# Optimization experiments

Hardware: AMD Instinct MI355X
Metric: run time of the kernel (lower is better)

The kernel has to match this reference:

```python
import jax, jax.numpy as jnp
import numpy as np

K_NBR = 128        # PyG radius(max_num_neighbors=128)
NEG_FILL = -1e9    # mask value for max-aggregation over invalid neighbors


def fps(pos, m):
    # Farthest point sampling on pos [N,2] -> [m] int32 indices (start at 0).
    n = pos.shape[0]
    def step(carry, _):
        min_d2, last = carry
        d2 = jnp.sum((pos - pos[last]) ** 2, axis=-1)
        min_d2 = jnp.minimum(min_d2, d2)
        nxt = jnp.argmax(min_d2).astype(jnp.int32)
        return (min_d2, nxt), nxt
    init = (jnp.full((n,), 1e10, pos.dtype), jnp.int32(0))
    _, idxs = jax.lax.scan(step, init, None, length=m - 1)
    return jnp.concatenate([jnp.zeros((1,), jnp.int32), idxs])


def set_abstraction(x, pos, ratio, r, W, b):
    # x [B,N,C], pos [B,N,2]. FPS centers, radius neighbors (<=K), PointNetConv
    # message = Linear(cat[x_j, pos_j - pos_i]) (PyG MLP with one layer and
    # plain_last=True is a bare Linear), then max-aggregate per center.
    B, N, C = x.shape
    m = int(N * ratio)
    idx = jax.vmap(lambda p: fps(p, m))(pos)                         # [B,m]
    ctr = jnp.take_along_axis(pos, idx[..., None], axis=1)           # [B,m,2]
    d2 = jnp.sum((ctr[:, :, None, :] - pos[:, None, :, :]) ** 2, -1)  # [B,m,N]
    k = min(K_NBR, N)
    neg_d2, nbr = jax.lax.top_k(-d2, k)                              # [B,m,k]
    valid = (-neg_d2) <= r * r                                       # in-radius mask
    gather = jax.vmap(lambda a, i: a[i])                             # per-sample fancy index
    x_j = gather(x, nbr)                                             # [B,m,k,C]
    rel = gather(pos, nbr) - ctr[:, :, None, :]                      # [B,m,k,2]
    msg = jnp.concatenate([x_j, rel], axis=-1) @ W + b               # [B,m,k,F]
    msg = jnp.where(valid[..., None], msg, NEG_FILL)
    return jnp.max(msg, axis=2), ctr                                 # [B,m,F], [B,m,2]


def encoder(x, zones_ids, lf_W1, lf_b1, lf_W2, lf_b2, c1_W, c1_b, c2_W, c2_b, c3_W, c3_b):
    lf = jnp.tanh(jnp.tanh(x @ lf_W1 + lf_b1) @ lf_W2 + lf_b2)       # [B,N,64]
    h = jnp.concatenate([lf, zones_ids], axis=-1)                    # [B,N,65]
    h, pos = set_abstraction(h, x, 0.5, 0.5, c1_W, c1_b)             # [B,N/2,64]
    h, pos = set_abstraction(h, pos, 0.25, 1.0, c2_W, c2_b)          # [B,N/8,128]
    g = jnp.concatenate([h, pos], axis=-1) @ c3_W + c3_b             # [B,N/8,1024]
    gf = jnp.max(g, axis=1, keepdims=True)                           # global max pool -> [B,1,1024]
    return lf, gf


def setup_inputs():
    key = jax.random.key(0)
    ks = jax.random.split(key, 12)
    B, N = 4, 4096
    def lin(kw, kb, fi, fo):
        return (jax.random.normal(kw, (fi, fo), jnp.float32) / np.sqrt(fi),
                jax.random.normal(kb, (fo,), jnp.float32) * 0.01)
    x = jax.random.normal(ks[0], (B, N, 2), jnp.float32) * 4.0  # spread so ball(r) holds <128 pts
    zones_ids = jax.random.uniform(ks[1], (B, N, 1), jnp.float32)
    lf_W1, lf_b1 = lin(ks[2], ks[3], 2, 64)
    lf_W2, lf_b2 = lin(ks[4], ks[5], 64, 64)
    c1_W, c1_b = lin(ks[6], ks[7], 67, 64)
    c2_W, c2_b = lin(ks[8], ks[9], 66, 128)
    c3_W, c3_b = lin(ks[10], ks[11], 130, 1024)
    return {"x": x, "zones_ids": zones_ids, "lf_W1": lf_W1, "lf_b1": lf_b1,
            "lf_W2": lf_W2, "lf_b2": lf_b2, "c1_W": c1_W, "c1_b": c1_b,
            "c2_W": c2_W, "c2_b": c2_b, "c3_W": c3_W, "c3_b": c3_b}


def reference(x, zones_ids, lf_W1, lf_b1, lf_W2, lf_b2, c1_W, c1_b, c2_W, c2_b, c3_W, c3_b):
    return encoder(x, zones_ids, lf_W1, lf_b1, lf_W2, lf_b2,
                   c1_W, c1_b, c2_W, c2_b, c3_W, c3_b)
```

## Files before the change

### kernel.cpp

```cpp
#include <hip/hip_runtime.h>


constexpr int BB = 4;
constexpr int NN = 4096;
constexpr int M1 = 2048;
constexpr int M2 = 512;

typedef float v2f __attribute__((ext_vector_type(2)));

__device__ __forceinline__ float d2_exact(float dx, float dy) {
    return __fadd_rn(__fmul_rn(dx, dx), __fmul_rn(dy, dy));
}

template<int CTRL>
__device__ __forceinline__ unsigned long long dpp64z(unsigned long long v) {
    unsigned lo = (unsigned)__builtin_amdgcn_update_dpp(0, (int)(unsigned)v, CTRL, 0xF, 0xF, true);
    unsigned hi = (unsigned)__builtin_amdgcn_update_dpp(0, (int)(unsigned)(v >> 32), CTRL, 0xF, 0xF, true);
    return ((unsigned long long)hi << 32) | (unsigned long long)lo;
}
template<int CTRL>
__device__ __forceinline__ void pairc(unsigned long long& t1, unsigned long long& t2) {
    unsigned long long o1 = dpp64z<CTRL>(t1);
    unsigned long long o2 = dpp64z<CTRL>(t2);
    bool g = o1 > t1;
    unsigned long long m1 = g ? o1 : t1;
    unsigned long long sm = g ? t1 : o1;
    unsigned long long cn = g ? o2 : t2;
    t2 = cn > sm ? cn : sm;
    t1 = m1;
}

template<int M, int PPT>
__device__ __forceinline__ void fps_core(
    const float2* __restrict__ src, const float2* __restrict__ PTSl,
    float2* __restrict__ centl, uint4 (&slk)[2][4],
    int tid, int lane, int wv)
{
#pragma clang fp contract(off)
    constexpr int PP2 = PPT / 2;
    v2f px2[PP2], py2[PP2], md2[PP2];
#pragma unroll
    for (int k = 0; k < PP2; ++k) {
        float2 a = src[tid + (2 * k) * 256];
        float2 b = src[tid + (2 * k + 1) * 256];
        px2[k] = (v2f){a.x, b.x};
        py2[k] = (v2f){a.y, b.y};
        md2[k] = (v2f){1e10f, 1e10f};
    }
    float2 c0 = src[0];
    if (tid == 0) centl[0] = c0;

    unsigned baseu = 0xFFFFFFFFu - (unsigned)tid;
    float c1x = c0.x, c1y = c0.y, c2x = 0.0f, c2y = 0.0f;
    bool two = false;
    int it = 1;
    unsigned rc = 0;
    while (it < M) {
        int par = (int)(rc & 1u); ++rc;
        v2f vcx = (v2f){c1x, c1x}, vcy = (v2f){c1y, c1y};
#pragma unroll
        for (int k = 0; k < PP2; ++k) {
            v2f dx = px2[k] - vcx, dy = py2[k] - vcy;
            v2f d2 = (dx * dx) + (dy * dy);
            md2[k] = __builtin_elementwise_min(md2[k], d2);
        }
        if (two) {
            v2f wcx = (v2f){c2x, c2x}, wcy = (v2f){c2y, c2y};
#pragma unroll
            for (int k = 0; k < PP2; ++k) {
                v2f dx = px2[k] - wcx, dy = py2[k] - wcy;
                v2f d2 = (dx * dx) + (dy * dy);
                md2[k] = __builtin_elementwise_min(md2[k], d2);
            }
        }
        float t1f = -1.0f, t2f = -1.0f;
        unsigned i1 = 0u, i2 = 0u;
#pragma unroll
        for (int s = 0; s < PPT; ++s) {
            float mq = (s & 1) ? md2[s >> 1].y : md2[s >> 1].x;
            unsigned io = baseu - (unsigned)(s * 256);
            bool g1 = mq > t1f;
            bool g2 = mq > t2f;
            t2f = g1 ? t1f : (g2 ? mq : t2f);
            i2  = g1 ? i1  : (g2 ? io : i2);
            t1f = g1 ? mq : t1f;
            i1  = g1 ? io : i1;
        }
        unsigned long long t1 =
            ((unsigned long long)__float_as_uint(t1f) << 32) | (unsigned long long)i1;
        unsigned long long t2 =
            ((unsigned long long)__float_as_uint(t2f) << 32) | (unsigned long long)i2;
        pairc<0x111>(t1, t2); pairc<0x112>(t1, t2); pairc<0x114>(t1, t2);
        pairc<0x118>(t1, t2); pairc<0x142>(t1, t2); pairc<0x143>(t1, t2);
        if (lane == 63)
            slk[par][wv] = make_uint4((unsigned)t1, (unsigned)(t1 >> 32),
                                      (unsigned)t2, (unsigned)(t2 >> 32));
        __syncthreads();
        uint4 e = slk[par][lane & 3];
        unsigned long long a1 = ((unsigned long long)e.y << 32) | (unsigned long long)e.x;
        unsigned long long a2 = ((unsigned long long)e.w << 32) | (unsigned long long)e.z;
        pairc<0xB1>(a1, a2);
        pairc<0x4E>(a1, a2);
        int jw = (int)(0xFFFFFFFFu - (unsigned)a1);
        int jr = (int)(0xFFFFFFFFu - (unsigned)a2);
        float mdr = __uint_as_float((unsigned)(a2 >> 32));
        float2 wpt = PTSl[jw];
        float2 rpt = PTSl[jr];
        float ddx = rpt.x - wpt.x, ddy = rpt.y - wpt.y;
        float dd = (ddx * ddx) + (ddy * ddy);
        bool dbl = (it + 1 < M) && (dd >= mdr);
        if (tid == 0) { centl[it] = wpt; if (dbl) centl[it + 1] = rpt; }
        c1x = wpt.x; c1y = wpt.y; c2x = rpt.x; c2y = rpt.y;
        two = dbl;
        it += dbl ? 2 : 1;
    }
}

__global__ __launch_bounds__(256, 1) void k_fps_lf(
    const float2* __restrict__ pos, float* __restrict__ p1out,
    float* __restrict__ p2out,
    const float* __restrict__ zones,
    const float* __restrict__ W1, const float* __restrict__ b1,
    const float* __restrict__ W2, const float* __restrict__ b2,
    const float* __restrict__ c1W, const float* __restrict__ c1b,
    float* __restrict__ out_lf, float* __restrict__ y1)
{
    __shared__ float2 PTS[NN];
    __shared__ float2 cent1[M1];
    __shared__ float2 cent2[M2];
    __shared__ uint4 slk[2][4];
    int tid = threadIdx.x, lane = tid & 63, wv = tid >> 6;

    if (blockIdx.x >= (unsigned)BB) {
        float* sh = (float*)PTS;
        float* sl = sh + 256;
        int p = tid >> 6, f = tid & 63;
        size_t pt = (size_t)(blockIdx.x - BB) * 4 + p;
        float2 xv = pos[pt];
        float hid = tanhf(xv.x * W1[f] + xv.y * W1[64 + f] + b1[f]);
        sh[p * 64 + f] = hid;
        __syncthreads();
        float acc = b2[f];
#pragma unroll
        for (int c = 0; c < 64; ++c) acc += sh[p * 64 + c] * W2[c * 64 + f];
        float lf = tanhf(acc);
        sl[p * 64 + f] = lf;
        out_lf[pt * 64 + f] = lf;
        __syncthreads();
        float acc2 = c1b[f] + zones[pt] * c1W[64 * 64 + f]
                   + xv.x * c1W[65 * 64 + f] + xv.y * c1W[66 * 64 + f];
#pragma unroll
        for (int c = 0; c < 64; ++c) acc2 += sl[p * 64 + c] * c1W[c * 64 + f];
        y1[pt * 64 + f] = acc2;
        return;
    }

    const float2* p = pos + (size_t)blockIdx.x * NN;
    for (int i = tid; i < NN; i += 256) PTS[i] = p[i];
    __syncthreads();

    fps_core<M1, NN / 256>(p, PTS, cent1, slk, tid, lane, wv);
    __syncthreads();
    float2* o1 = (float2*)(p1out + (size_t)blockIdx.x * M1 * 2);
    for (int i = tid; i < M1; i += 256) o1[i] = cent1[i];

    fps_core<M2, M1 / 256>(cent1, cent1, cent2, slk, tid, lane, wv);
    __syncthreads();
    float2* o2 = (float2*)(p2out + (size_t)blockIdx.x * M2 * 2);
    for (int i = tid; i < M2; i += 256) o2[i] = cent2[i];
}

__global__ __launch_bounds__(256) void k_sa(
    const float2* __restrict__ candpos, const float* __restrict__ y,
    const float* __restrict__ ctr, const float* __restrict__ W,
    int NP, int F, int relrow, float r2, float* __restrict__ hout)
{
    __shared__ int cnt;
    __shared__ int list[4096];
    int tid = threadIdx.x;
    int b = blockIdx.y;
    size_t crow = (size_t)b * gridDim.x + blockIdx.x;
    if (tid == 0) cnt = 0;
    __syncthreads();
    float cx = ctr[crow * 2], cy = ctr[crow * 2 + 1];
    const float2* cp = candpos + (size_t)b * NP;
    for (int j = tid; j < NP; j += 256) {
        float2 pj = cp[j];
        float d2 = d2_exact(pj.x - cx, pj.y - cy);
        if (d2 <= r2) { int t = atomicAdd(&cnt, 1); list[t] = j; }
    }
    __syncthreads();
    int n = cnt;
    for (int f = tid; f < F; f += 256) {
        float m = -3.0e38f;
        for (int t = 0; t < n; ++t)
            m = fmaxf(m, y[((size_t)b * NP + list[t]) * F + f]);
        float ct = cx * W[(size_t)relrow * F + f] + cy * W[(size_t)(relrow + 1) * F + f];
        hout[crow * F + f] = m - ct;
    }
}

__global__ __launch_bounds__(128) void k_y2(
    const float* __restrict__ h1, const float* __restrict__ p1,
    const float* __restrict__ W, const float* __restrict__ bb,
    float* __restrict__ y2)
{
    __shared__ float sh[64];
    size_t row = blockIdx.x;
    int f = threadIdx.x;
    if (f < 64) sh[f] = h1[row * 64 + f];
    __syncthreads();
    float acc = bb[f] + p1[row * 2] * W[64 * 128 + f]
              + p1[row * 2 + 1] * W[65 * 128 + f];
#pragma unroll
    for (int c = 0; c < 64; ++c) acc += sh[c] * W[c * 128 + f];
    y2[row * 128 + f] = acc;
}

__global__ __launch_bounds__(256) void k_g(
    const float* __restrict__ h2, const float* __restrict__ p2,
    const float* __restrict__ W3, const float* __restrict__ b3,
    float* __restrict__ part)
{
    int f = blockIdx.x * 256 + threadIdx.x;
    int b = blockIdx.z;
    int i0 = blockIdx.y * 8;
    float acc[8];
    float bbv = b3[f];
#pragma unroll
    for (int ii = 0; ii < 8; ++ii) acc[ii] = bbv;
    const float* hrow = h2 + ((size_t)b * M2 + i0) * 128;
    for (int c = 0; c < 128; ++c) {
        float w = W3[(size_t)c * 1024 + f];
#pragma unroll
        for (int ii = 0; ii < 8; ++ii) acc[ii] += hrow[ii * 128 + c] * w;
    }
    float wx = W3[(size_t)128 * 1024 + f];
    float wy = W3[(size_t)129 * 1024 + f];
    const float* prow = p2 + ((size_t)b * M2 + i0) * 2;
    float m = -3.0e38f;
#pragma unroll
    for (int ii = 0; ii < 8; ++ii) {
        float g = acc[ii] + prow[ii * 2] * wx + prow[ii * 2 + 1] * wy;
        m = fmaxf(m, g);
    }
    part[((size_t)b * 64 + blockIdx.y) * 1024 + f] = m;
}

__global__ __launch_bounds__(256) void k_gmax(const float* __restrict__ part,
                                              float* __restrict__ outg)
{
    int f = blockIdx.x * 256 + threadIdx.x;
    int b = f >> 10, fl = f & 1023;
    float m = -3.0e38f;
#pragma unroll 8
    for (int ig = 0; ig < 64; ++ig)
        m = fmaxf(m, part[((size_t)b * 64 + ig) * 1024 + fl]);
    outg[f] = m;
}

extern "C" void kernel_launch(void* const* d_in, const int* in_sizes, int n_in,
                              void* d_out, int out_size, void* d_ws, size_t ws_size,
                              hipStream_t stream)
{
    const float* x    = (const float*)d_in[0];
    const float* zon  = (const float*)d_in[1];
    const float* lfW1 = (const float*)d_in[2];
    const float* lfb1 = (const float*)d_in[3];
    const float* lfW2 = (const float*)d_in[4];
    const float* lfb2 = (const float*)d_in[5];
    const float* c1W  = (const float*)d_in[6];
    const float* c1b  = (const float*)d_in[7];
    const float* c2W  = (const float*)d_in[8];
    const float* c2b  = (const float*)d_in[9];
    const float* c3W  = (const float*)d_in[10];
    const float* c3b  = (const float*)d_in[11];
    float* out = (float*)d_out;

    char* w = (char*)d_ws;
    float* big = (float*)w;                    w += (size_t)BB * NN * 64 * 4;
    float* p1  = (float*)w;                    w += (size_t)BB * M1 * 2 * 4;
    float* h1  = (float*)w;                    w += (size_t)BB * M1 * 64 * 4;
    float* p2  = (float*)w;                    w += (size_t)BB * M2 * 2 * 4;
    float* h2  = (float*)w;                    w += (size_t)BB * M2 * 128 * 4;
    float* y1 = big, * y2 = big, * part = big;

    k_fps_lf<<<BB + BB * NN / 4, 256, 0, stream>>>(
        (const float2*)x, p1, p2, zon, lfW1, lfb1, lfW2, lfb2, c1W, c1b, out, y1);
    k_sa<<<dim3(M1, BB), 256, 0, stream>>>((const float2*)x, y1, p1, c1W,
                                           NN, 64, 65, 0.25f, h1);
    k_y2<<<BB * M1, 128, 0, stream>>>(h1, p1, c2W, c2b, y2);
    k_sa<<<dim3(M2, BB), 256, 0, stream>>>((const float2*)p1, y2, p2, c2W,
                                           M1, 128, 64, 1.0f, h2);
    k_g<<<dim3(4, 64, BB), 256, 0, stream>>>(h2, p2, c3W, c3b, part);
    k_gmax<<<16, 256, 0, stream>>>(part, out + (size_t)BB * NN * 64);
}
```

Baseline: 1.528 ms.

## Overlap second-level FPS with first set-abstraction in a combined kernel

The second farthest-point-sampling pass is moved out of the first kernel, which previously ran both FPS levels serially on BB blocks, and into a new kernel. In that kernel BB blocks run FPS2 while the remaining blocks perform the level-1 radius search and max aggregation, replacing the separate k_sa launch. The serial FPS2 latency can then hide behind SA1 work instead of extending the critical path. The cost is a larger shared-memory footprint per block in the merged kernel, which may lower occupancy for the SA1 blocks, and the FPS blocks now sit alongside thousands of SA blocks.

```diff
diff --git a/kernel.cpp b/kernel.cpp
--- a/kernel.cpp
+++ b/kernel.cpp
@@ -116,9 +116,8 @@
     }
 }
 
-__global__ __launch_bounds__(256, 1) void k_fps_lf(
+__global__ __launch_bounds__(256, 1) void k_fps1(
     const float2* __restrict__ pos, float* __restrict__ p1out,
-    float* __restrict__ p2out,
     const float* __restrict__ zones,
     const float* __restrict__ W1, const float* __restrict__ b1,
     const float* __restrict__ W2, const float* __restrict__ b2,
@@ -127,7 +126,6 @@
 {
     __shared__ float2 PTS[NN];
     __shared__ float2 cent1[M1];
-    __shared__ float2 cent2[M2];
     __shared__ uint4 slk[2][4];
     int tid = threadIdx.x, lane = tid & 63, wv = tid >> 6;
 
@@ -163,11 +161,52 @@
     __syncthreads();
     float2* o1 = (float2*)(p1out + (size_t)blockIdx.x * M1 * 2);
     for (int i = tid; i < M1; i += 256) o1[i] = cent1[i];
-
-    fps_core<M2, M1 / 256>(cent1, cent1, cent2, slk, tid, lane, wv);
-    __syncthreads();
-    float2* o2 = (float2*)(p2out + (size_t)blockIdx.x * M2 * 2);
-    for (int i = tid; i < M2; i += 256) o2[i] = cent2[i];
+}
+
+__global__ __launch_bounds__(256) void k_fps2_sa1(
+    const float2* __restrict__ x, const float* __restrict__ p1,
+    const float* __restrict__ y1, const float* __restrict__ c1W,
+    float* __restrict__ p2out, float* __restrict__ h1)
+{
+    __shared__ float2 PTS2[M1];
+    __shared__ float2 cent2[M2];
+    __shared__ uint4 slk[2][4];
+    __shared__ int cnt;
+    __shared__ int list[NN];
+    int tid = threadIdx.x, lane = tid & 63, wv = tid >> 6;
+
+    if (blockIdx.x < (unsigned)BB) {
+        const float2* p1b = (const float2*)(p1 + (size_t)blockIdx.x * M1 * 2);
+        for (int i = tid; i < M1; i += 256) PTS2[i] = p1b[i];
+        __syncthreads();
+        fps_core<M2, M1 / 256>(PTS2, PTS2, cent2, slk, tid, lane, wv);
+        __syncthreads();
+        float2* o2 = (float2*)(p2out + (size_t)blockIdx.x * M2 * 2);
+        for (int i = tid; i < M2; i += 256) o2[i] = cent2[i];
+        return;
+    }
+
+    int idx = (int)blockIdx.x - BB;
+    int b = idx >> 11;
+    size_t crow = (size_t)idx;
+    if (tid == 0) cnt = 0;
+    __syncthreads();
+    float cx = p1[crow * 2], cy = p1[crow * 2 + 1];
+    const float2* cp = x + (size_t)b * NN;
+    for (int j = tid; j < NN; j += 256) {
+        float2 pj = cp[j];
+        float d2 = d2_exact(pj.x - cx, pj.y - cy);
+        if (d2 <= 0.25f) { int t = atomicAdd(&cnt, 1); list[t] = j; }
+    }
+    __syncthreads();
+    int n = cnt;
+    for (int f = tid; f < 64; f += 256) {
+        float m = -3.0e38f;
+        for (int t = 0; t < n; ++t)
+            m = fmaxf(m, y1[((size_t)b * NN + list[t]) * 64 + f]);
+        float ct = cx * c1W[(size_t)65 * 64 + f] + cy * c1W[(size_t)66 * 64 + f];
+        h1[crow * 64 + f] = m - ct;
+    }
 }
 
 __global__ __launch_bounds__(256) void k_sa(
@@ -285,10 +324,10 @@
     float* h2  = (float*)w;                    w += (size_t)BB * M2 * 128 * 4;
     float* y1 = big, * y2 = big, * part = big;
 
-    k_fps_lf<<<BB + BB * NN / 4, 256, 0, stream>>>(
-        (const float2*)x, p1, p2, zon, lfW1, lfb1, lfW2, lfb2, c1W, c1b, out, y1);
-    k_sa<<<dim3(M1, BB), 256, 0, stream>>>((const float2*)x, y1, p1, c1W,
-                                           NN, 64, 65, 0.25f, h1);
+    k_fps1<<<BB + BB * NN / 4, 256, 0, stream>>>(
+        (const float2*)x, p1, zon, lfW1, lfb1, lfW2, lfb2, c1W, c1b, out, y1);
+    k_fps2_sa1<<<BB + BB * M1, 256, 0, stream>>>(
+        (const float2*)x, p1, y1, c1W, p2, h1);
     k_y2<<<BB * M1, 128, 0, stream>>>(h1, p1, c2W, c2b, y2);
     k_sa<<<dim3(M2, BB), 256, 0, stream>>>((const float2*)p1, y2, p2, c2W,
                                            M1, 128, 64, 1.0f, h2);
```

Result: faster. 1.458 ms (-4.6%).
